# Kernel optimization log

Measured on AMD Instinct MI355X. Metric: run time of the kernel, lower is better.

Reference implementation:

```python
import jax, jax.numpy as jnp
from jax import lax
import numpy as np

B, T, IN, H, OUT = 1024, 512, 64, 128, 2
BN_EPS = 1e-5


def _gru_layer(x, w_ih, w_hh, b_ih, b_hh):
    # x: [B, T, F]; w_ih: [3H, F]; w_hh: [3H, H]; gate order = (r, z, n) as in PyTorch
    Bb = x.shape[0]
    Hh = w_hh.shape[1]
    xg = jnp.einsum('btf,gf->btg', x, w_ih) + b_ih  # precompute input gates [B, T, 3H]

    def step(h, xg_t):
        hg = h @ w_hh.T + b_hh                       # [B, 3H]
        xr, xz, xn = jnp.split(xg_t, 3, axis=-1)
        hr, hz, hn = jnp.split(hg, 3, axis=-1)
        r = jax.nn.sigmoid(xr + hr)
        z = jax.nn.sigmoid(xz + hz)
        n = jnp.tanh(xn + r * hn)
        h_new = (1.0 - z) * n + z * h
        return h_new, h_new

    h0 = jnp.zeros((Bb, Hh), dtype=x.dtype)
    _, ys = lax.scan(step, h0, jnp.swapaxes(xg, 0, 1))  # scan over time
    return jnp.swapaxes(ys, 0, 1)                        # [B, T, H]


def setup_inputs() -> dict:
    key = jax.random.key(0)
    ks = jax.random.split(key, 16)
    s_in = 1.0 / np.sqrt(H)  # PyTorch GRU init scale
    d = {
        'x': jax.random.normal(ks[0], (B, T, IN), dtype=jnp.float32),
        'w_ih0': jax.random.uniform(ks[1], (3 * H, IN), minval=-s_in, maxval=s_in),
        'w_hh0': jax.random.uniform(ks[2], (3 * H, H), minval=-s_in, maxval=s_in),
        'b_ih0': jax.random.uniform(ks[3], (3 * H,), minval=-s_in, maxval=s_in),
        'b_hh0': jax.random.uniform(ks[4], (3 * H,), minval=-s_in, maxval=s_in),
        'w_ih1': jax.random.uniform(ks[5], (3 * H, H), minval=-s_in, maxval=s_in),
        'w_hh1': jax.random.uniform(ks[6], (3 * H, H), minval=-s_in, maxval=s_in),
        'b_ih1': jax.random.uniform(ks[7], (3 * H,), minval=-s_in, maxval=s_in),
        'b_hh1': jax.random.uniform(ks[8], (3 * H,), minval=-s_in, maxval=s_in),
        'fc1_w': jax.random.normal(ks[9], (H // 2, H)) * 0.05,
        'fc1_b': jnp.zeros((H // 2,)),
        'fc2_w': jax.random.normal(ks[10], (OUT, H // 2)) * 0.05,
        'fc2_b': jnp.zeros((OUT,)),
        'bn_gamma': jnp.ones((H // 2,)),
        'bn_beta': jnp.zeros((H // 2,)),
        'bn_mean': jnp.zeros((H // 2,)),
        'bn_var': jnp.ones((H // 2,)),
    }
    return d


def reference(x, w_ih0, w_hh0, b_ih0, b_hh0, w_ih1, w_hh1, b_ih1, b_hh1,
              fc1_w, fc1_b, fc2_w, fc2_b, bn_gamma, bn_beta, bn_mean, bn_var):
    h1 = _gru_layer(x, w_ih0, w_hh0, b_ih0, b_hh0)   # [B, T, H]
    h2 = _gru_layer(h1, w_ih1, w_hh1, b_ih1, b_hh1)  # [B, T, H]
    out = h2[:, -1, :]                                # last timestep [B, H]
    # dropout = identity (eval mode)
    out = jax.nn.relu(out @ fc1_w.T + fc1_b)          # [B, H/2]
    out = (out - bn_mean) * jax.lax.rsqrt(bn_var + BN_EPS) * bn_gamma + bn_beta
    out = out @ fc2_w.T + fc2_b                       # [B, 2]
    return out
```

## Files before the change

kernel.cpp:

```cpp
#include <hip/hip_runtime.h>
#include <hip/hip_bf16.h>

namespace {

typedef _Float16 h16;
typedef _Float16 f16x8 __attribute__((ext_vector_type(8)));
typedef _Float16 f16x4 __attribute__((ext_vector_type(4)));
typedef _Float16 f16x2 __attribute__((ext_vector_type(2)));
typedef float    f32x4 __attribute__((ext_vector_type(4)));
typedef unsigned long long u64;

constexpr int T_SEQ = 512;
constexpr int B_SZ  = 1024;
constexpr int H_DIM = 128;
constexpr int ROWS  = 16;
constexpr int NT    = 512;
constexpr int NGRP  = B_SZ / ROWS;
constexpr int CHUNK = 32;

template <int INDIM, bool PROD>
__device__ void gru_body(char* smem_raw, float* headbuf,
                         const float* __restrict__ xin,
                         const float* __restrict__ w_ih,
                         const float* __restrict__ w_hh,
                         const float* __restrict__ b_ih,
                         const float* __restrict__ b_hh,
                         u64* __restrict__ h1q,
                         int* __restrict__ flag,
                         const float* __restrict__ fc1_w,
                         const float* __restrict__ fc1_b,
                         const float* __restrict__ fc2_w,
                         const float* __restrict__ fc2_b,
                         const float* __restrict__ gamma,
                         const float* __restrict__ beta,
                         const float* __restrict__ mean,
                         const float* __restrict__ var,
                         float* __restrict__ out,
                         const int g)
{
  constexpr int KSH  = H_DIM / 32;
  constexpr int KSX  = INDIM / 32;
  constexpr int ROWP = H_DIM + INDIM + 8;

  auto hx = reinterpret_cast<h16 (*)[ROWS][ROWP]>(smem_raw);

  const int tid = threadIdx.x;
  const int wv  = tid >> 6;
  const int ln  = tid & 63;
  const int q   = ln >> 4;
  const int lr  = ln & 15;
  const int r0  = g * ROWS;
  const int j0  = wv * 16 + q * 4;

  f16x8 wA[3][KSH], wB[3][KSX];
  #pragma unroll
  for (int p = 0; p < 3; ++p) {
    const int gr = p * H_DIM + wv * 16 + lr;
    #pragma unroll
    for (int ks = 0; ks < KSH; ++ks) {
      const float* pw = w_hh + (size_t)gr * H_DIM + ks * 32 + q * 8;
      const float4 v0 = *(const float4*)(pw);
      const float4 v1 = *(const float4*)(pw + 4);
      f16x8 f;
      f[0]=(h16)v0.x; f[1]=(h16)v0.y; f[2]=(h16)v0.z; f[3]=(h16)v0.w;
      f[4]=(h16)v1.x; f[5]=(h16)v1.y; f[6]=(h16)v1.z; f[7]=(h16)v1.w;
      wA[p][ks] = f;
    }
    #pragma unroll
    for (int ks = 0; ks < KSX; ++ks) {
      const float* pw = w_ih + (size_t)gr * INDIM + ks * 32 + q * 8;
      const float4 v0 = *(const float4*)(pw);
      const float4 v1 = *(const float4*)(pw + 4);
      f16x8 f;
      f[0]=(h16)v0.x; f[1]=(h16)v0.y; f[2]=(h16)v0.z; f[3]=(h16)v0.w;
      f[4]=(h16)v1.x; f[5]=(h16)v1.y; f[6]=(h16)v1.z; f[7]=(h16)v1.w;
      wB[p][ks] = f;
    }
  }

  f32x4 bR, bZ, bNx, bNh;
  {
    const float4 ir  = *(const float4*)&b_ih[j0];
    const float4 hr  = *(const float4*)&b_hh[j0];
    const float4 iz  = *(const float4*)&b_ih[H_DIM + j0];
    const float4 hz  = *(const float4*)&b_hh[H_DIM + j0];
    const float4 in_ = *(const float4*)&b_ih[2 * H_DIM + j0];
    const float4 hn  = *(const float4*)&b_hh[2 * H_DIM + j0];
    bR[0]=ir.x+hr.x; bR[1]=ir.y+hr.y; bR[2]=ir.z+hr.z; bR[3]=ir.w+hr.w;
    bZ[0]=iz.x+hz.x; bZ[1]=iz.y+hz.y; bZ[2]=iz.z+hz.z; bZ[3]=iz.w+hz.w;
    bNx[0]=in_.x; bNx[1]=in_.y; bNx[2]=in_.z; bNx[3]=in_.w;
    bNh[0]=hn.x;  bNh[1]=hn.y;  bNh[2]=hn.z;  bNh[3]=hn.w;
  }

  const int sr = tid >> 5;
  const int si = tid & 31;

  {
    f16x4 z; z[0]=z[1]=z[2]=z[3] = (h16)0.f;
    *(f16x4*)&hx[0][sr][si * 4] = z;
  }
  f16x4 h_old; h_old[0]=h_old[1]=h_old[2]=h_old[3] = (h16)0.f;

  auto load_h1 = [&](int t, f16x4& d) {
    const u64 bits = __hip_atomic_load(&h1q[((size_t)t * B_SZ + r0 + sr) * 32 + si],
                                       __ATOMIC_RELAXED, __HIP_MEMORY_SCOPE_AGENT);
    __builtin_memcpy(&d, &bits, 8);
  };

  f16x2 sA, sB;
  f16x4 cA, cB;
  if constexpr (PROD) {
    const float2 v0 = *(const float2*)(xin + ((size_t)(r0 + sr) * T_SEQ + 0) * 64 + si * 2);
    f16x2 s0; s0[0] = (h16)v0.x; s0[1] = (h16)v0.y;
    *(f16x2*)&hx[0][sr][H_DIM + si * 2] = s0;
    const float2 v1 = *(const float2*)(xin + ((size_t)(r0 + sr) * T_SEQ + 1) * 64 + si * 2);
    sA[0] = (h16)v1.x; sA[1] = (h16)v1.y;
  } else {
    while (__hip_atomic_load(flag, __ATOMIC_ACQUIRE, __HIP_MEMORY_SCOPE_AGENT) < 1)
      __builtin_amdgcn_s_sleep(2);
    f16x4 s0; load_h1(0, s0);
    *(f16x4*)&hx[0][sr][H_DIM + si * 4] = s0;
    load_h1(1, cA);
  }
  __syncthreads();

  auto gates = [&](const f32x4& aR, const f32x4& aZ, const f32x4& aNx2, const f32x4& aNh2,
                   f16x4& nv4, float* hnv) {
    #pragma unroll
    for (int i = 0; i < 4; ++i) {
      const float rg = __builtin_amdgcn_rcpf(1.f + __expf(-aR[i]));
      const float zg = __builtin_amdgcn_rcpf(1.f + __expf(-aZ[i]));
      const float na = aNx2[i] + rg * aNh2[i];
      const float e2 = __expf(2.f * na);
      const float ng = 1.f - 2.f * __builtin_amdgcn_rcpf(e2 + 1.f);
      const float ho = (float)h_old[i];
      const float hn = ng + zg * (ho - ng);
      hnv[i] = hn;
      nv4[i] = (h16)hn;
    }
    h_old = nv4;
  };

  auto mfma_all = [&](const f16x8* bh, const f16x8* bx,
                      f32x4& aR, f32x4& aZ, f32x4& aNh2, f32x4& aNx2) {
    aR = bR; aZ = bZ; aNh2 = bNh; aNx2 = bNx;
    #pragma unroll
    for (int ks = 0; ks < KSH; ++ks) {
      aR   = __builtin_amdgcn_mfma_f32_16x16x32_f16(wA[0][ks], bh[ks], aR, 0, 0, 0);
      aZ   = __builtin_amdgcn_mfma_f32_16x16x32_f16(wA[1][ks], bh[ks], aZ, 0, 0, 0);
      aNh2 = __builtin_amdgcn_mfma_f32_16x16x32_f16(wA[2][ks], bh[ks], aNh2, 0, 0, 0);
    }
    #pragma unroll
    for (int ks = 0; ks < KSX; ++ks) {
      aR   = __builtin_amdgcn_mfma_f32_16x16x32_f16(wB[0][ks], bx[ks], aR, 0, 0, 0);
      aZ   = __builtin_amdgcn_mfma_f32_16x16x32_f16(wB[1][ks], bx[ks], aZ, 0, 0, 0);
      aNx2 = __builtin_amdgcn_mfma_f32_16x16x32_f16(wB[2][ks], bx[ks], aNx2, 0, 0, 0);
    }
  };

  if constexpr (PROD) {
    auto pstep = [&](int t, int cur, f16x2& s_use, f16x2& s_load) {
      f16x8 bh[KSH], bx[KSX];
      #pragma unroll
      for (int ks = 0; ks < KSH; ++ks) bh[ks] = *(const f16x8*)&hx[cur][lr][ks * 32 + q * 8];
      #pragma unroll
      for (int ks = 0; ks < KSX; ++ks) bx[ks] = *(const f16x8*)&hx[cur][lr][H_DIM + ks * 32 + q * 8];

      {
        const int tt = (t + 2 < T_SEQ) ? t + 2 : T_SEQ - 1;
        const float2 v = *(const float2*)(xin + ((size_t)(r0 + sr) * T_SEQ + tt) * 64 + si * 2);
        s_load[0] = (h16)v.x; s_load[1] = (h16)v.y;
      }

      f32x4 aR, aZ, aNh2, aNx2;
      mfma_all(bh, bx, aR, aZ, aNh2, aNx2);

      f16x4 nv4; float hnv[4];
      gates(aR, aZ, aNx2, aNh2, nv4, hnv);

      u64 bits; __builtin_memcpy(&bits, &nv4, 8);
      __hip_atomic_store(&h1q[((size_t)t * B_SZ + r0 + lr) * 32 + (j0 >> 2)], bits,
                         __ATOMIC_RELAXED, __HIP_MEMORY_SCOPE_AGENT);

      *(f16x4*)&hx[cur ^ 1][lr][j0] = nv4;
      *(f16x2*)&hx[cur ^ 1][sr][H_DIM + si * 2] = s_use;

      if ((t & (CHUNK - 1)) == CHUNK - 1) __threadfence();
      __syncthreads();
      if (((t & (CHUNK - 1)) == CHUNK - 1) && tid == 0)
        __hip_atomic_store(flag, (t + 1) / CHUNK, __ATOMIC_RELEASE, __HIP_MEMORY_SCOPE_AGENT);
    };

    #pragma unroll 1
    for (int t = 0; t < T_SEQ; t += 2) {
      pstep(t,     0, sA, sB);
      pstep(t + 1, 1, sB, sA);
    }
  } else {
    auto cstep = [&](int t, int cur, f16x4& s_use, f16x4& s_load) {
      f16x8 bh[KSH], bx[KSX];
      #pragma unroll
      for (int ks = 0; ks < KSH; ++ks) bh[ks] = *(const f16x8*)&hx[cur][lr][ks * 32 + q * 8];
      #pragma unroll
      for (int ks = 0; ks < KSX; ++ks) bx[ks] = *(const f16x8*)&hx[cur][lr][H_DIM + ks * 32 + q * 8];

      if (t + 2 < T_SEQ) {
        if (((t + 2) & (CHUNK - 1)) == 0) {
          const int need = (t + 2) / CHUNK + 1;
          while (__hip_atomic_load(flag, __ATOMIC_ACQUIRE, __HIP_MEMORY_SCOPE_AGENT) < need)
            __builtin_amdgcn_s_sleep(2);
        }
        load_h1(t + 2, s_load);
      }

      f32x4 aR, aZ, aNh2, aNx2;
      mfma_all(bh, bx, aR, aZ, aNh2, aNx2);

      f16x4 nv4; float hnv[4];
      gates(aR, aZ, aNx2, aNh2, nv4, hnv);

      *(f16x4*)&hx[cur ^ 1][lr][j0] = nv4;
      if (t + 1 < T_SEQ) *(f16x4*)&hx[cur ^ 1][sr][H_DIM + si * 4] = s_use;

      if (t == T_SEQ - 1) {
        float* h2f = headbuf;
        float* act = headbuf + 16 * 128;
        #pragma unroll
        for (int i = 0; i < 4; ++i) h2f[lr * 128 + j0 + i] = hnv[i];
        __syncthreads();
        {
          const int row = tid >> 5;
          const float* hr = &h2f[row * 128];
          #pragma unroll
          for (int half = 0; half < 2; ++half) {
            const int j = (tid & 31) + half * 32;
            float s = fc1_b[j];
            const float4* wr = (const float4*)(fc1_w + (size_t)j * H_DIM);
            #pragma unroll
            for (int k4 = 0; k4 < H_DIM / 4; ++k4) {
              const float4 w = wr[k4];
              const float4 h = ((const float4*)hr)[k4];
              s += w.x * h.x + w.y * h.y + w.z * h.z + w.w * h.w;
            }
            s = fmaxf(s, 0.f);
            s = (s - mean[j]) * rsqrtf(var[j] + 1e-5f) * gamma[j] + beta[j];
            act[row * 64 + j] = s;
          }
        }
        __syncthreads();
        if (tid < 32) {
          const int r = tid >> 1, o = tid & 1;
          float s = fc2_b[o];
          #pragma unroll
          for (int k = 0; k < 64; ++k) s += fc2_w[(size_t)o * 64 + k] * act[r * 64 + k];
          out[(size_t)(r0 + r) * 2 + o] = s;
        }
      }
      __syncthreads();
    };

    #pragma unroll 1
    for (int t = 0; t < T_SEQ; t += 2) {
      cstep(t,     0, cA, cB);
      cstep(t + 1, 1, cB, cA);
    }
  }
}

__global__ __launch_bounds__(NT, 1)
void gru_fused(const float* __restrict__ x,
               const float* __restrict__ w_ih0, const float* __restrict__ w_hh0,
               const float* __restrict__ b_ih0, const float* __restrict__ b_hh0,
               const float* __restrict__ w_ih1, const float* __restrict__ w_hh1,
               const float* __restrict__ b_ih1, const float* __restrict__ b_hh1,
               u64* __restrict__ h1q, int* __restrict__ flags,
               const float* __restrict__ fc1_w, const float* __restrict__ fc1_b,
               const float* __restrict__ fc2_w, const float* __restrict__ fc2_b,
               const float* __restrict__ gamma, const float* __restrict__ beta,
               const float* __restrict__ mean,  const float* __restrict__ var,
               float* __restrict__ out)
{
  __shared__ __align__(16) char smem[(size_t)2 * ROWS * (H_DIM + H_DIM + 8) * sizeof(h16)];
  __shared__ __align__(16) float headbuf[16 * 128 + 16 * 64];
  const int bid = blockIdx.x;
  if (bid < NGRP)
    gru_body<64, true>(smem, headbuf, x, w_ih0, w_hh0, b_ih0, b_hh0, h1q, &flags[bid],
                       nullptr, nullptr, nullptr, nullptr, nullptr, nullptr, nullptr, nullptr,
                       nullptr, bid);
  else
    gru_body<128, false>(smem, headbuf, nullptr, w_ih1, w_hh1, b_ih1, b_hh1, h1q,
                         &flags[bid - NGRP], fc1_w, fc1_b, fc2_w, fc2_b, gamma, beta,
                         mean, var, out, bid - NGRP);
}

}

extern "C" void kernel_launch(void* const* d_in, const int* in_sizes, int n_in,
                              void* d_out, int out_size, void* d_ws, size_t ws_size,
                              hipStream_t stream) {
  const float* x     = (const float*)d_in[0];
  const float* w_ih0 = (const float*)d_in[1];
  const float* w_hh0 = (const float*)d_in[2];
  const float* b_ih0 = (const float*)d_in[3];
  const float* b_hh0 = (const float*)d_in[4];
  const float* w_ih1 = (const float*)d_in[5];
  const float* w_hh1 = (const float*)d_in[6];
  const float* b_ih1 = (const float*)d_in[7];
  const float* b_hh1 = (const float*)d_in[8];
  const float* fc1_w = (const float*)d_in[9];
  const float* fc1_b = (const float*)d_in[10];
  const float* fc2_w = (const float*)d_in[11];
  const float* fc2_b = (const float*)d_in[12];
  const float* gamma = (const float*)d_in[13];
  const float* beta  = (const float*)d_in[14];
  const float* mean  = (const float*)d_in[15];
  const float* var   = (const float*)d_in[16];
  float* out = (float*)d_out;

  char* ws = (char*)d_ws;
  const size_t h1_bytes = (size_t)T_SEQ * B_SZ * H_DIM * sizeof(h16);
  const size_t fl_bytes = (size_t)NGRP * sizeof(int);
  if (ws_size < h1_bytes + fl_bytes) return;

  u64* h1q   = (u64*)ws;
  int* flags = (int*)(ws + h1_bytes);

  hipMemsetAsync(flags, 0, fl_bytes, stream);
  gru_fused<<<dim3(2 * NGRP), dim3(NT), 0, stream>>>(
      x, w_ih0, w_hh0, b_ih0, b_hh0, w_ih1, w_hh1, b_ih1, b_hh1, h1q, flags,
      fc1_w, fc1_b, fc2_w, fc2_b, gamma, beta, mean, var, out);
}
```

Before: 663.7 us.

## Move layer-1 input projection into producer blocks with ring-buffered gate queue

The layer-0 producer now also computes layer 1's input-gate projection (W_ih1·h1) from its fresh hidden state. It streams the three fp16 gate vectors through a bounded ring buffer in global memory, with back-pressure flags from the consumer. The consumer's serial critical path shrinks to only the W_hh1 recurrent MFMAs plus the gates, which balances work between the two pipeline stages. In exchange the producer does roughly double the MFMA work per step, global traffic per step triples (three gate vectors instead of one hidden vector), and the producer can stall on the ring-full wait.

```diff
diff --git a/kernel.cpp b/kernel.cpp
--- a/kernel.cpp
+++ b/kernel.cpp
@@ -10,38 +10,40 @@
 typedef float    f32x4 __attribute__((ext_vector_type(4)));
 typedef unsigned long long u64;
 
-constexpr int T_SEQ = 512;
-constexpr int B_SZ  = 1024;
-constexpr int H_DIM = 128;
-constexpr int ROWS  = 16;
-constexpr int NT    = 512;
-constexpr int NGRP  = B_SZ / ROWS;
-constexpr int CHUNK = 32;
-
-template <int INDIM, bool PROD>
-__device__ void gru_body(char* smem_raw, float* headbuf,
-                         const float* __restrict__ xin,
-                         const float* __restrict__ w_ih,
-                         const float* __restrict__ w_hh,
-                         const float* __restrict__ b_ih,
-                         const float* __restrict__ b_hh,
-                         u64* __restrict__ h1q,
-                         int* __restrict__ flag,
-                         const float* __restrict__ fc1_w,
-                         const float* __restrict__ fc1_b,
-                         const float* __restrict__ fc2_w,
-                         const float* __restrict__ fc2_b,
-                         const float* __restrict__ gamma,
-                         const float* __restrict__ beta,
-                         const float* __restrict__ mean,
-                         const float* __restrict__ var,
-                         float* __restrict__ out,
-                         const int g)
+constexpr int T_SEQ  = 512;
+constexpr int B_SZ   = 1024;
+constexpr int H_DIM  = 128;
+constexpr int ROWS   = 16;
+constexpr int NT     = 512;
+constexpr int NGRP   = B_SZ / ROWS;
+constexpr int CHUNK  = 32;
+constexpr int RING_C = 4;
+constexpr int RING_T = RING_C * CHUNK;
+
+__device__ __forceinline__ size_t xg_idx(int p, int t, int g, int tid) {
+  return ((size_t)(p * RING_T + (t & (RING_T - 1))) * NGRP + g) * 512 + tid;
+}
+
+__device__ __forceinline__ void spin_ge(int* f, int v) {
+  while (__hip_atomic_load(f, __ATOMIC_ACQUIRE, __HIP_MEMORY_SCOPE_AGENT) < v)
+    __builtin_amdgcn_s_sleep(2);
+}
+
+__device__ void prod_body(char* smem_raw,
+                          const float* __restrict__ xin,
+                          const float* __restrict__ w_ih0,
+                          const float* __restrict__ w_hh0,
+                          const float* __restrict__ b_ih0,
+                          const float* __restrict__ b_hh0,
+                          const float* __restrict__ w_ih1,
+                          const float* __restrict__ b_ih1,
+                          const float* __restrict__ b_hh1,
+                          u64* __restrict__ xgq,
+                          int* __restrict__ pflag, int* __restrict__ cflag,
+                          const int g)
 {
-  constexpr int KSH  = H_DIM / 32;
-  constexpr int KSX  = INDIM / 32;
-  constexpr int ROWP = H_DIM + INDIM + 8;
-
+  constexpr int KSH = 4, KSX = 2;
+  constexpr int ROWP = H_DIM + 64 + 8;
   auto hx = reinterpret_cast<h16 (*)[ROWS][ROWP]>(smem_raw);
 
   const int tid = threadIdx.x;
@@ -52,44 +54,49 @@
   const int r0  = g * ROWS;
   const int j0  = wv * 16 + q * 4;
 
-  f16x8 wA[3][KSH], wB[3][KSX];
+  auto ldw = [](const float* pw) {
+    const float4 v0 = *(const float4*)(pw);
+    const float4 v1 = *(const float4*)(pw + 4);
+    f16x8 f;
+    f[0]=(h16)v0.x; f[1]=(h16)v0.y; f[2]=(h16)v0.z; f[3]=(h16)v0.w;
+    f[4]=(h16)v1.x; f[5]=(h16)v1.y; f[6]=(h16)v1.z; f[7]=(h16)v1.w;
+    return f;
+  };
+
+  f16x8 wA0[3][KSH], wB0[3][KSX], wI1[3][KSH];
   #pragma unroll
   for (int p = 0; p < 3; ++p) {
     const int gr = p * H_DIM + wv * 16 + lr;
     #pragma unroll
     for (int ks = 0; ks < KSH; ++ks) {
-      const float* pw = w_hh + (size_t)gr * H_DIM + ks * 32 + q * 8;
-      const float4 v0 = *(const float4*)(pw);
-      const float4 v1 = *(const float4*)(pw + 4);
-      f16x8 f;
-      f[0]=(h16)v0.x; f[1]=(h16)v0.y; f[2]=(h16)v0.z; f[3]=(h16)v0.w;
-      f[4]=(h16)v1.x; f[5]=(h16)v1.y; f[6]=(h16)v1.z; f[7]=(h16)v1.w;
-      wA[p][ks] = f;
-    }
-    #pragma unroll
-    for (int ks = 0; ks < KSX; ++ks) {
-      const float* pw = w_ih + (size_t)gr * INDIM + ks * 32 + q * 8;
-      const float4 v0 = *(const float4*)(pw);
-      const float4 v1 = *(const float4*)(pw + 4);
-      f16x8 f;
-      f[0]=(h16)v0.x; f[1]=(h16)v0.y; f[2]=(h16)v0.z; f[3]=(h16)v0.w;
-      f[4]=(h16)v1.x; f[5]=(h16)v1.y; f[6]=(h16)v1.z; f[7]=(h16)v1.w;
-      wB[p][ks] = f;
-    }
-  }
-
-  f32x4 bR, bZ, bNx, bNh;
-  {
-    const float4 ir  = *(const float4*)&b_ih[j0];
-    const float4 hr  = *(const float4*)&b_hh[j0];
-    const float4 iz  = *(const float4*)&b_ih[H_DIM + j0];
-    const float4 hz  = *(const float4*)&b_hh[H_DIM + j0];
-    const float4 in_ = *(const float4*)&b_ih[2 * H_DIM + j0];
-    const float4 hn  = *(const float4*)&b_hh[2 * H_DIM + j0];
-    bR[0]=ir.x+hr.x; bR[1]=ir.y+hr.y; bR[2]=ir.z+hr.z; bR[3]=ir.w+hr.w;
-    bZ[0]=iz.x+hz.x; bZ[1]=iz.y+hz.y; bZ[2]=iz.z+hz.z; bZ[3]=iz.w+hz.w;
-    bNx[0]=in_.x; bNx[1]=in_.y; bNx[2]=in_.z; bNx[3]=in_.w;
-    bNh[0]=hn.x;  bNh[1]=hn.y;  bNh[2]=hn.z;  bNh[3]=hn.w;
+      wA0[p][ks] = ldw(w_hh0 + (size_t)gr * H_DIM + ks * 32 + q * 8);
+      wI1[p][ks] = ldw(w_ih1 + (size_t)gr * H_DIM + ks * 32 + q * 8);
+    }
+    #pragma unroll
+    for (int ks = 0; ks < KSX; ++ks)
+      wB0[p][ks] = ldw(w_ih0 + (size_t)gr * 64 + ks * 32 + q * 8);
+  }
+
+  f32x4 bR0, bZ0, bNx0, bNh0, xbR, xbZ, xbN;
+  {
+    const float4 ir  = *(const float4*)&b_ih0[j0];
+    const float4 hr  = *(const float4*)&b_hh0[j0];
+    const float4 iz  = *(const float4*)&b_ih0[H_DIM + j0];
+    const float4 hz  = *(const float4*)&b_hh0[H_DIM + j0];
+    const float4 in_ = *(const float4*)&b_ih0[2 * H_DIM + j0];
+    const float4 hn  = *(const float4*)&b_hh0[2 * H_DIM + j0];
+    bR0[0]=ir.x+hr.x; bR0[1]=ir.y+hr.y; bR0[2]=ir.z+hr.z; bR0[3]=ir.w+hr.w;
+    bZ0[0]=iz.x+hz.x; bZ0[1]=iz.y+hz.y; bZ0[2]=iz.z+hz.z; bZ0[3]=iz.w+hz.w;
+    bNx0[0]=in_.x; bNx0[1]=in_.y; bNx0[2]=in_.z; bNx0[3]=in_.w;
+    bNh0[0]=hn.x;  bNh0[1]=hn.y;  bNh0[2]=hn.z;  bNh0[3]=hn.w;
+    const float4 jr  = *(const float4*)&b_ih1[j0];
+    const float4 kr  = *(const float4*)&b_hh1[j0];
+    const float4 jz  = *(const float4*)&b_ih1[H_DIM + j0];
+    const float4 kz  = *(const float4*)&b_hh1[H_DIM + j0];
+    const float4 jn  = *(const float4*)&b_ih1[2 * H_DIM + j0];
+    xbR[0]=jr.x+kr.x; xbR[1]=jr.y+kr.y; xbR[2]=jr.z+kr.z; xbR[3]=jr.w+kr.w;
+    xbZ[0]=jz.x+kz.x; xbZ[1]=jz.y+kz.y; xbZ[2]=jz.z+kz.z; xbZ[3]=jz.w+kz.w;
+    xbN[0]=jn.x; xbN[1]=jn.y; xbN[2]=jn.z; xbN[3]=jn.w;
   }
 
   const int sr = tid >> 5;
@@ -101,36 +108,205 @@
   }
   f16x4 h_old; h_old[0]=h_old[1]=h_old[2]=h_old[3] = (h16)0.f;
 
-  auto load_h1 = [&](int t, f16x4& d) {
-    const u64 bits = __hip_atomic_load(&h1q[((size_t)t * B_SZ + r0 + sr) * 32 + si],
-                                       __ATOMIC_RELAXED, __HIP_MEMORY_SCOPE_AGENT);
-    __builtin_memcpy(&d, &bits, 8);
-  };
-
   f16x2 sA, sB;
-  f16x4 cA, cB;
-  if constexpr (PROD) {
+  {
     const float2 v0 = *(const float2*)(xin + ((size_t)(r0 + sr) * T_SEQ + 0) * 64 + si * 2);
     f16x2 s0; s0[0] = (h16)v0.x; s0[1] = (h16)v0.y;
     *(f16x2*)&hx[0][sr][H_DIM + si * 2] = s0;
     const float2 v1 = *(const float2*)(xin + ((size_t)(r0 + sr) * T_SEQ + 1) * 64 + si * 2);
     sA[0] = (h16)v1.x; sA[1] = (h16)v1.y;
-  } else {
-    while (__hip_atomic_load(flag, __ATOMIC_ACQUIRE, __HIP_MEMORY_SCOPE_AGENT) < 1)
-      __builtin_amdgcn_s_sleep(2);
-    f16x4 s0; load_h1(0, s0);
-    *(f16x4*)&hx[0][sr][H_DIM + si * 4] = s0;
-    load_h1(1, cA);
   }
   __syncthreads();
 
-  auto gates = [&](const f32x4& aR, const f32x4& aZ, const f32x4& aNx2, const f32x4& aNh2,
-                   f16x4& nv4, float* hnv) {
+  auto pstep = [&](int t, int cur, f16x2& s_use, f16x2& s_load) {
+    if ((t & (CHUNK - 1)) == 0 && t >= RING_T)
+      spin_ge(cflag, t / CHUNK - (RING_C - 1));
+
+    f16x8 bh[KSH], bx[KSX];
+    #pragma unroll
+    for (int ks = 0; ks < KSH; ++ks) bh[ks] = *(const f16x8*)&hx[cur][lr][ks * 32 + q * 8];
+    #pragma unroll
+    for (int ks = 0; ks < KSX; ++ks) bx[ks] = *(const f16x8*)&hx[cur][lr][H_DIM + ks * 32 + q * 8];
+
+    {
+      const int tt = (t + 2 < T_SEQ) ? t + 2 : T_SEQ - 1;
+      const float2 v = *(const float2*)(xin + ((size_t)(r0 + sr) * T_SEQ + tt) * 64 + si * 2);
+      s_load[0] = (h16)v.x; s_load[1] = (h16)v.y;
+    }
+
+    f32x4 aR = bR0, aZ = bZ0, aNh = bNh0, aNx = bNx0;
+    f32x4 xR = xbR, xZ = xbZ, xN = xbN;
+    #pragma unroll
+    for (int ks = 0; ks < KSH; ++ks) {
+      aR  = __builtin_amdgcn_mfma_f32_16x16x32_f16(wA0[0][ks], bh[ks], aR,  0, 0, 0);
+      aZ  = __builtin_amdgcn_mfma_f32_16x16x32_f16(wA0[1][ks], bh[ks], aZ,  0, 0, 0);
+      aNh = __builtin_amdgcn_mfma_f32_16x16x32_f16(wA0[2][ks], bh[ks], aNh, 0, 0, 0);
+      xR  = __builtin_amdgcn_mfma_f32_16x16x32_f16(wI1[0][ks], bh[ks], xR,  0, 0, 0);
+      xZ  = __builtin_amdgcn_mfma_f32_16x16x32_f16(wI1[1][ks], bh[ks], xZ,  0, 0, 0);
+      xN  = __builtin_amdgcn_mfma_f32_16x16x32_f16(wI1[2][ks], bh[ks], xN,  0, 0, 0);
+    }
+    #pragma unroll
+    for (int c = 0; c < KSX; ++c) {
+      aR  = __builtin_amdgcn_mfma_f32_16x16x32_f16(wB0[0][c], bx[c], aR,  0, 0, 0);
+      aZ  = __builtin_amdgcn_mfma_f32_16x16x32_f16(wB0[1][c], bx[c], aZ,  0, 0, 0);
+      aNx = __builtin_amdgcn_mfma_f32_16x16x32_f16(wB0[2][c], bx[c], aNx, 0, 0, 0);
+    }
+
+    f16x4 nv4;
+    {
+      float hnv[4];
+      #pragma unroll
+      for (int i = 0; i < 4; ++i) {
+        const float rg = __builtin_amdgcn_rcpf(1.f + __expf(-aR[i]));
+        const float zg = __builtin_amdgcn_rcpf(1.f + __expf(-aZ[i]));
+        const float na = aNx[i] + rg * aNh[i];
+        const float e2 = __expf(2.f * na);
+        const float ng = 1.f - 2.f * __builtin_amdgcn_rcpf(e2 + 1.f);
+        const float ho = (float)h_old[i];
+        const float hn = ng + zg * (ho - ng);
+        hnv[i] = hn;
+        nv4[i] = (h16)hn;
+      }
+      h_old = nv4;
+    }
+
+    if (t > 0) {
+      f16x4 xr4, xz4, xn4;
+      #pragma unroll
+      for (int i = 0; i < 4; ++i) { xr4[i]=(h16)xR[i]; xz4[i]=(h16)xZ[i]; xn4[i]=(h16)xN[i]; }
+      u64 b0, b1, b2;
+      __builtin_memcpy(&b0, &xr4, 8); __builtin_memcpy(&b1, &xz4, 8); __builtin_memcpy(&b2, &xn4, 8);
+      __hip_atomic_store(&xgq[xg_idx(0, t - 1, g, tid)], b0, __ATOMIC_RELAXED, __HIP_MEMORY_SCOPE_AGENT);
+      __hip_atomic_store(&xgq[xg_idx(1, t - 1, g, tid)], b1, __ATOMIC_RELAXED, __HIP_MEMORY_SCOPE_AGENT);
+      __hip_atomic_store(&xgq[xg_idx(2, t - 1, g, tid)], b2, __ATOMIC_RELAXED, __HIP_MEMORY_SCOPE_AGENT);
+    }
+
+    *(f16x4*)&hx[cur ^ 1][lr][j0] = nv4;
+    *(f16x2*)&hx[cur ^ 1][sr][H_DIM + si * 2] = s_use;
+
+    if ((t & (CHUNK - 1)) == 0 && t > 0) __threadfence();
+    __syncthreads();
+    if ((t & (CHUNK - 1)) == 0 && t > 0 && tid == 0)
+      __hip_atomic_store(pflag, t / CHUNK, __ATOMIC_RELEASE, __HIP_MEMORY_SCOPE_AGENT);
+  };
+
+  #pragma unroll 1
+  for (int t = 0; t < T_SEQ; t += 2) {
+    pstep(t,     0, sA, sB);
+    pstep(t + 1, 1, sB, sA);
+  }
+  {
+    f16x8 bh[KSH];
+    #pragma unroll
+    for (int ks = 0; ks < KSH; ++ks) bh[ks] = *(const f16x8*)&hx[0][lr][ks * 32 + q * 8];
+    f32x4 xR = xbR, xZ = xbZ, xN = xbN;
+    #pragma unroll
+    for (int ks = 0; ks < KSH; ++ks) {
+      xR = __builtin_amdgcn_mfma_f32_16x16x32_f16(wI1[0][ks], bh[ks], xR, 0, 0, 0);
+      xZ = __builtin_amdgcn_mfma_f32_16x16x32_f16(wI1[1][ks], bh[ks], xZ, 0, 0, 0);
+      xN = __builtin_amdgcn_mfma_f32_16x16x32_f16(wI1[2][ks], bh[ks], xN, 0, 0, 0);
+    }
+    f16x4 xr4, xz4, xn4;
+    #pragma unroll
+    for (int i = 0; i < 4; ++i) { xr4[i]=(h16)xR[i]; xz4[i]=(h16)xZ[i]; xn4[i]=(h16)xN[i]; }
+    u64 b0, b1, b2;
+    __builtin_memcpy(&b0, &xr4, 8); __builtin_memcpy(&b1, &xz4, 8); __builtin_memcpy(&b2, &xn4, 8);
+    __hip_atomic_store(&xgq[xg_idx(0, 511, g, tid)], b0, __ATOMIC_RELAXED, __HIP_MEMORY_SCOPE_AGENT);
+    __hip_atomic_store(&xgq[xg_idx(1, 511, g, tid)], b1, __ATOMIC_RELAXED, __HIP_MEMORY_SCOPE_AGENT);
+    __hip_atomic_store(&xgq[xg_idx(2, 511, g, tid)], b2, __ATOMIC_RELAXED, __HIP_MEMORY_SCOPE_AGENT);
+    __threadfence();
+    __syncthreads();
+    if (tid == 0)
+      __hip_atomic_store(pflag, T_SEQ / CHUNK, __ATOMIC_RELEASE, __HIP_MEMORY_SCOPE_AGENT);
+  }
+}
+
+__device__ void cons_body(char* smem_raw, float* headbuf,
+                          const float* __restrict__ w_hh1,
+                          const float* __restrict__ b_hh1,
+                          const u64* __restrict__ xgq,
+                          int* __restrict__ pflag, int* __restrict__ cflag,
+                          const float* __restrict__ fc1_w, const float* __restrict__ fc1_b,
+                          const float* __restrict__ fc2_w, const float* __restrict__ fc2_b,
+                          const float* __restrict__ gamma, const float* __restrict__ beta,
+                          const float* __restrict__ mean,  const float* __restrict__ var,
+                          float* __restrict__ out, const int g)
+{
+  constexpr int KSH = 4;
+  constexpr int ROWP = H_DIM + 8;
+  auto hx = reinterpret_cast<h16 (*)[ROWS][ROWP]>(smem_raw);
+
+  const int tid = threadIdx.x;
+  const int wv  = tid >> 6;
+  const int ln  = tid & 63;
+  const int q   = ln >> 4;
+  const int lr  = ln & 15;
+  const int r0  = g * ROWS;
+  const int j0  = wv * 16 + q * 4;
+
+  auto ldw = [](const float* pw) {
+    const float4 v0 = *(const float4*)(pw);
+    const float4 v1 = *(const float4*)(pw + 4);
+    f16x8 f;
+    f[0]=(h16)v0.x; f[1]=(h16)v0.y; f[2]=(h16)v0.z; f[3]=(h16)v0.w;
+    f[4]=(h16)v1.x; f[5]=(h16)v1.y; f[6]=(h16)v1.z; f[7]=(h16)v1.w;
+    return f;
+  };
+
+  f16x8 wA1[3][KSH];
+  #pragma unroll
+  for (int p = 0; p < 3; ++p) {
+    const int gr = p * H_DIM + wv * 16 + lr;
+    #pragma unroll
+    for (int ks = 0; ks < KSH; ++ks)
+      wA1[p][ks] = ldw(w_hh1 + (size_t)gr * H_DIM + ks * 32 + q * 8);
+  }
+  f32x4 bNh1;
+  {
+    const float4 hn = *(const float4*)&b_hh1[2 * H_DIM + j0];
+    bNh1[0]=hn.x; bNh1[1]=hn.y; bNh1[2]=hn.z; bNh1[3]=hn.w;
+  }
+
+  {
+    f16x4 z; z[0]=z[1]=z[2]=z[3] = (h16)0.f;
+    *(f16x4*)&hx[0][tid >> 5][(tid & 31) * 4] = z;
+  }
+  f16x4 h_old; h_old[0]=h_old[1]=h_old[2]=h_old[3] = (h16)0.f;
+
+  auto load_xg = [&](int t, f16x4* d) {
+    const u64 b0 = __hip_atomic_load(&xgq[xg_idx(0, t, g, tid)], __ATOMIC_RELAXED, __HIP_MEMORY_SCOPE_AGENT);
+    const u64 b1 = __hip_atomic_load(&xgq[xg_idx(1, t, g, tid)], __ATOMIC_RELAXED, __HIP_MEMORY_SCOPE_AGENT);
+    const u64 b2 = __hip_atomic_load(&xgq[xg_idx(2, t, g, tid)], __ATOMIC_RELAXED, __HIP_MEMORY_SCOPE_AGENT);
+    __builtin_memcpy(&d[0], &b0, 8);
+    __builtin_memcpy(&d[1], &b1, 8);
+    __builtin_memcpy(&d[2], &b2, 8);
+  };
+
+  spin_ge(pflag, 1);
+  f16x4 X0[3], X1[3];
+  load_xg(0, X0);
+  load_xg(1, X1);
+  __syncthreads();
+
+  auto cstep = [&](int t, int cur, f16x4* Xuse) {
+    f16x8 bh2[KSH];
+    #pragma unroll
+    for (int ks = 0; ks < KSH; ++ks) bh2[ks] = *(const f16x8*)&hx[cur][lr][ks * 32 + q * 8];
+
+    f32x4 rR = (f32x4)(0.f), rZ = (f32x4)(0.f), rNh = bNh1;
+    #pragma unroll
+    for (int ks = 0; ks < KSH; ++ks) {
+      rR  = __builtin_amdgcn_mfma_f32_16x16x32_f16(wA1[0][ks], bh2[ks], rR,  0, 0, 0);
+      rZ  = __builtin_amdgcn_mfma_f32_16x16x32_f16(wA1[1][ks], bh2[ks], rZ,  0, 0, 0);
+      rNh = __builtin_amdgcn_mfma_f32_16x16x32_f16(wA1[2][ks], bh2[ks], rNh, 0, 0, 0);
+    }
+
+    f16x4 nv4; float hnv[4];
     #pragma unroll
     for (int i = 0; i < 4; ++i) {
-      const float rg = __builtin_amdgcn_rcpf(1.f + __expf(-aR[i]));
-      const float zg = __builtin_amdgcn_rcpf(1.f + __expf(-aZ[i]));
-      const float na = aNx2[i] + rg * aNh2[i];
+      const float rg = __builtin_amdgcn_rcpf(1.f + __expf(-((float)Xuse[0][i] + rR[i])));
+      const float zg = __builtin_amdgcn_rcpf(1.f + __expf(-((float)Xuse[1][i] + rZ[i])));
+      const float na = (float)Xuse[2][i] + rg * rNh[i];
       const float e2 = __expf(2.f * na);
       const float ng = 1.f - 2.f * __builtin_amdgcn_rcpf(e2 + 1.f);
       const float ho = (float)h_old[i];
@@ -139,131 +315,57 @@
       nv4[i] = (h16)hn;
     }
     h_old = nv4;
-  };
-
-  auto mfma_all = [&](const f16x8* bh, const f16x8* bx,
-                      f32x4& aR, f32x4& aZ, f32x4& aNh2, f32x4& aNx2) {
-    aR = bR; aZ = bZ; aNh2 = bNh; aNx2 = bNx;
-    #pragma unroll
-    for (int ks = 0; ks < KSH; ++ks) {
-      aR   = __builtin_amdgcn_mfma_f32_16x16x32_f16(wA[0][ks], bh[ks], aR, 0, 0, 0);
-      aZ   = __builtin_amdgcn_mfma_f32_16x16x32_f16(wA[1][ks], bh[ks], aZ, 0, 0, 0);
-      aNh2 = __builtin_amdgcn_mfma_f32_16x16x32_f16(wA[2][ks], bh[ks], aNh2, 0, 0, 0);
-    }
-    #pragma unroll
-    for (int ks = 0; ks < KSX; ++ks) {
-      aR   = __builtin_amdgcn_mfma_f32_16x16x32_f16(wB[0][ks], bx[ks], aR, 0, 0, 0);
-      aZ   = __builtin_amdgcn_mfma_f32_16x16x32_f16(wB[1][ks], bx[ks], aZ, 0, 0, 0);
-      aNx2 = __builtin_amdgcn_mfma_f32_16x16x32_f16(wB[2][ks], bx[ks], aNx2, 0, 0, 0);
-    }
-  };
-
-  if constexpr (PROD) {
-    auto pstep = [&](int t, int cur, f16x2& s_use, f16x2& s_load) {
-      f16x8 bh[KSH], bx[KSX];
+    *(f16x4*)&hx[cur ^ 1][lr][j0] = nv4;
+
+    if (t + 2 < T_SEQ) {
+      if (((t + 2) & (CHUNK - 1)) == 0)
+        spin_ge(pflag, (t + 2) / CHUNK + 1);
+      load_xg(t + 2, Xuse);
+    }
+
+    if (t == T_SEQ - 1) {
+      float* h2f = headbuf;
+      float* act = headbuf + 16 * 128;
       #pragma unroll
-      for (int ks = 0; ks < KSH; ++ks) bh[ks] = *(const f16x8*)&hx[cur][lr][ks * 32 + q * 8];
-      #pragma unroll
-      for (int ks = 0; ks < KSX; ++ks) bx[ks] = *(const f16x8*)&hx[cur][lr][H_DIM + ks * 32 + q * 8];
-
+      for (int i = 0; i < 4; ++i) h2f[lr * 128 + j0 + i] = hnv[i];
+      __syncthreads();
       {
-        const int tt = (t + 2 < T_SEQ) ? t + 2 : T_SEQ - 1;
-        const float2 v = *(const float2*)(xin + ((size_t)(r0 + sr) * T_SEQ + tt) * 64 + si * 2);
-        s_load[0] = (h16)v.x; s_load[1] = (h16)v.y;
-      }
-
-      f32x4 aR, aZ, aNh2, aNx2;
-      mfma_all(bh, bx, aR, aZ, aNh2, aNx2);
-
-      f16x4 nv4; float hnv[4];
-      gates(aR, aZ, aNx2, aNh2, nv4, hnv);
-
-      u64 bits; __builtin_memcpy(&bits, &nv4, 8);
-      __hip_atomic_store(&h1q[((size_t)t * B_SZ + r0 + lr) * 32 + (j0 >> 2)], bits,
-                         __ATOMIC_RELAXED, __HIP_MEMORY_SCOPE_AGENT);
-
-      *(f16x4*)&hx[cur ^ 1][lr][j0] = nv4;
-      *(f16x2*)&hx[cur ^ 1][sr][H_DIM + si * 2] = s_use;
-
-      if ((t & (CHUNK - 1)) == CHUNK - 1) __threadfence();
-      __syncthreads();
-      if (((t & (CHUNK - 1)) == CHUNK - 1) && tid == 0)
-        __hip_atomic_store(flag, (t + 1) / CHUNK, __ATOMIC_RELEASE, __HIP_MEMORY_SCOPE_AGENT);
-    };
-
-    #pragma unroll 1
-    for (int t = 0; t < T_SEQ; t += 2) {
-      pstep(t,     0, sA, sB);
-      pstep(t + 1, 1, sB, sA);
-    }
-  } else {
-    auto cstep = [&](int t, int cur, f16x4& s_use, f16x4& s_load) {
-      f16x8 bh[KSH], bx[KSX];
-      #pragma unroll
-      for (int ks = 0; ks < KSH; ++ks) bh[ks] = *(const f16x8*)&hx[cur][lr][ks * 32 + q * 8];
-      #pragma unroll
-      for (int ks = 0; ks < KSX; ++ks) bx[ks] = *(const f16x8*)&hx[cur][lr][H_DIM + ks * 32 + q * 8];
-
-      if (t + 2 < T_SEQ) {
-        if (((t + 2) & (CHUNK - 1)) == 0) {
-          const int need = (t + 2) / CHUNK + 1;
-          while (__hip_atomic_load(flag, __ATOMIC_ACQUIRE, __HIP_MEMORY_SCOPE_AGENT) < need)
-            __builtin_amdgcn_s_sleep(2);
-        }
-        load_h1(t + 2, s_load);
-      }
-
-      f32x4 aR, aZ, aNh2, aNx2;
-      mfma_all(bh, bx, aR, aZ, aNh2, aNx2);
-
-      f16x4 nv4; float hnv[4];
-      gates(aR, aZ, aNx2, aNh2, nv4, hnv);
-
-      *(f16x4*)&hx[cur ^ 1][lr][j0] = nv4;
-      if (t + 1 < T_SEQ) *(f16x4*)&hx[cur ^ 1][sr][H_DIM + si * 4] = s_use;
-
-      if (t == T_SEQ - 1) {
-        float* h2f = headbuf;
-        float* act = headbuf + 16 * 128;
+        const int row = tid >> 5;
+        const float* hr = &h2f[row * 128];
         #pragma unroll
-        for (int i = 0; i < 4; ++i) h2f[lr * 128 + j0 + i] = hnv[i];
-        __syncthreads();
-        {
-          const int row = tid >> 5;
-          const float* hr = &h2f[row * 128];
+        for (int half = 0; half < 2; ++half) {
+          const int j = (tid & 31) + half * 32;
+          float s = fc1_b[j];
+          const float4* wr = (const float4*)(fc1_w + (size_t)j * H_DIM);
           #pragma unroll
-          for (int half = 0; half < 2; ++half) {
-            const int j = (tid & 31) + half * 32;
-            float s = fc1_b[j];
-            const float4* wr = (const float4*)(fc1_w + (size_t)j * H_DIM);
-            #pragma unroll
-            for (int k4 = 0; k4 < H_DIM / 4; ++k4) {
-              const float4 w = wr[k4];
-              const float4 h = ((const float4*)hr)[k4];
-              s += w.x * h.x + w.y * h.y + w.z * h.z + w.w * h.w;
-            }
-            s = fmaxf(s, 0.f);
-            s = (s - mean[j]) * rsqrtf(var[j] + 1e-5f) * gamma[j] + beta[j];
-            act[row * 64 + j] = s;
+          for (int k4 = 0; k4 < H_DIM / 4; ++k4) {
+            const float4 w = wr[k4];
+            const float4 h = ((const float4*)hr)[k4];
+            s += w.x * h.x + w.y * h.y + w.z * h.z + w.w * h.w;
           }
-        }
-        __syncthreads();
-        if (tid < 32) {
-          const int r = tid >> 1, o = tid & 1;
-          float s = fc2_b[o];
-          #pragma unroll
-          for (int k = 0; k < 64; ++k) s += fc2_w[(size_t)o * 64 + k] * act[r * 64 + k];
-          out[(size_t)(r0 + r) * 2 + o] = s;
+          s = fmaxf(s, 0.f);
+          s = (s - mean[j]) * rsqrtf(var[j] + 1e-5f) * gamma[j] + beta[j];
+          act[row * 64 + j] = s;
         }
       }
       __syncthreads();
-    };
-
-    #pragma unroll 1
-    for (int t = 0; t < T_SEQ; t += 2) {
-      cstep(t,     0, cA, cB);
-      cstep(t + 1, 1, cB, cA);
-    }
+      if (tid < 32) {
+        const int r = tid >> 1, o = tid & 1;
+        float s = fc2_b[o];
+        #pragma unroll
+        for (int k = 0; k < 64; ++k) s += fc2_w[(size_t)o * 64 + k] * act[r * 64 + k];
+        out[(size_t)(r0 + r) * 2 + o] = s;
+      }
+    }
+    __syncthreads();
+    if ((t & (CHUNK - 1)) == CHUNK - 1 && tid == 0)
+      __hip_atomic_store(cflag, t / CHUNK + 1, __ATOMIC_RELEASE, __HIP_MEMORY_SCOPE_AGENT);
+  };
+
+  #pragma unroll 1
+  for (int t = 0; t < T_SEQ; t += 2) {
+    cstep(t,     0, X0);
+    cstep(t + 1, 1, X1);
   }
 }
 
@@ -273,24 +375,23 @@
                const float* __restrict__ b_ih0, const float* __restrict__ b_hh0,
                const float* __restrict__ w_ih1, const float* __restrict__ w_hh1,
                const float* __restrict__ b_ih1, const float* __restrict__ b_hh1,
-               u64* __restrict__ h1q, int* __restrict__ flags,
+               u64* __restrict__ xgq, int* __restrict__ pflags, int* __restrict__ cflags,
                const float* __restrict__ fc1_w, const float* __restrict__ fc1_b,
                const float* __restrict__ fc2_w, const float* __restrict__ fc2_b,
                const float* __restrict__ gamma, const float* __restrict__ beta,
                const float* __restrict__ mean,  const float* __restrict__ var,
                float* __restrict__ out)
 {
-  __shared__ __align__(16) char smem[(size_t)2 * ROWS * (H_DIM + H_DIM + 8) * sizeof(h16)];
+  __shared__ __align__(16) char smem[(size_t)2 * ROWS * (H_DIM + 64 + 8) * sizeof(h16)];
   __shared__ __align__(16) float headbuf[16 * 128 + 16 * 64];
   const int bid = blockIdx.x;
   if (bid < NGRP)
-    gru_body<64, true>(smem, headbuf, x, w_ih0, w_hh0, b_ih0, b_hh0, h1q, &flags[bid],
-                       nullptr, nullptr, nullptr, nullptr, nullptr, nullptr, nullptr, nullptr,
-                       nullptr, bid);
+    prod_body(smem, x, w_ih0, w_hh0, b_ih0, b_hh0, w_ih1, b_ih1, b_hh1,
+              xgq, &pflags[bid], &cflags[bid], bid);
   else
-    gru_body<128, false>(smem, headbuf, nullptr, w_ih1, w_hh1, b_ih1, b_hh1, h1q,
-                         &flags[bid - NGRP], fc1_w, fc1_b, fc2_w, fc2_b, gamma, beta,
-                         mean, var, out, bid - NGRP);
+    cons_body(smem, headbuf, w_hh1, b_hh1, xgq,
+              &pflags[bid - NGRP], &cflags[bid - NGRP],
+              fc1_w, fc1_b, fc2_w, fc2_b, gamma, beta, mean, var, out, bid - NGRP);
 }
 
 }
@@ -318,15 +419,16 @@
   float* out = (float*)d_out;
 
   char* ws = (char*)d_ws;
-  const size_t h1_bytes = (size_t)T_SEQ * B_SZ * H_DIM * sizeof(h16);
-  const size_t fl_bytes = (size_t)NGRP * sizeof(int);
-  if (ws_size < h1_bytes + fl_bytes) return;
-
-  u64* h1q   = (u64*)ws;
-  int* flags = (int*)(ws + h1_bytes);
-
-  hipMemsetAsync(flags, 0, fl_bytes, stream);
+  const size_t xg_bytes = (size_t)3 * RING_T * NGRP * 512 * sizeof(u64);
+  const size_t fl_bytes = (size_t)2 * NGRP * sizeof(int);
+  if (ws_size < xg_bytes + fl_bytes) return;
+
+  u64* xgq    = (u64*)ws;
+  int* pflags = (int*)(ws + xg_bytes);
+  int* cflags = pflags + NGRP;
+
+  hipMemsetAsync(pflags, 0, fl_bytes, stream);
   gru_fused<<<dim3(2 * NGRP), dim3(NT), 0, stream>>>(
-      x, w_ih0, w_hh0, b_ih0, b_hh0, w_ih1, w_hh1, b_ih1, b_hh1, h1q, flags,
-      fc1_w, fc1_b, fc2_w, fc2_b, gamma, beta, mean, var, out);
-}
+      x, w_ih0, w_hh0, b_ih0, b_hh0, w_ih1, w_hh1, b_ih1, b_hh1,
+      xgq, pflags, cflags, fc1_w, fc1_b, fc2_w, fc2_b, gamma, beta, mean, var, out);
+}
```

New measurement: 819.3 us. +23.4%, slower.
